# Kernel optimization log

Hardware: AMD Instinct MI355X
Metric: run time of the kernel (lower is better)

Reference implementation:

```python
import jax, jax.numpy as jnp
import numpy as np
from jax import lax

DIM = 256
MOTION = 128
HEADS = 8
HID = int(DIM * 3.0)
EPS = 1e-5


def std_ln(x, w, b):
    # standard nn.LayerNorm: biased var, /sqrt(var+eps)
    mean = x.mean(-1, keepdims=True)
    var = jnp.var(x, axis=-1, keepdims=True)
    return w * (x - mean) / jnp.sqrt(var + EPS) + b


def custom_ln(x, w, b):
    # repo's custom LayerNorm: UNBIASED std (ddof=1) and divide by (std+eps)
    mean = x.mean(-1, keepdims=True)
    std = jnp.std(x, axis=-1, ddof=1, keepdims=True)
    return w * (x - mean) / (std + EPS) + b


def setup_inputs() -> dict:
    key = jax.random.key(0)
    ks = jax.random.split(key, 32)
    s = 0.02
    d = {}
    d['x'] = jax.random.normal(ks[0], (4, 16384, DIM), jnp.float32)
    d['cor'] = jax.random.uniform(ks[1], (4, 128, 128, 2), jnp.float32)
    # attention projections (qkv_bias=False)
    d['q_w'] = jax.random.normal(ks[2], (DIM, DIM), jnp.float32) * s
    d['kv_w'] = jax.random.normal(ks[3], (2 * DIM, DIM), jnp.float32) * s
    d['cor_w'] = jax.random.normal(ks[4], (MOTION, 2), jnp.float32) * s
    hd = DIM // HEADS
    md = MOTION // HEADS
    d['kln_w'] = jnp.ones((HEADS, 1, hd), jnp.float32)
    d['kln_b'] = jnp.zeros((HEADS, 1, hd), jnp.float32)
    d['vln_w'] = jnp.ones((HEADS, 1, hd), jnp.float32)
    d['vln_b'] = jnp.zeros((HEADS, 1, hd), jnp.float32)
    d['corln_w'] = jnp.ones((HEADS, 1, md), jnp.float32)
    d['corln_b'] = jnp.zeros((HEADS, 1, md), jnp.float32)
    d['op1_w'] = jax.random.normal(ks[5], (DIM, DIM), jnp.float32) * s
    d['op1_b'] = jnp.zeros((DIM,), jnp.float32)
    d['op2_w'] = jax.random.normal(ks[6], (DIM, DIM), jnp.float32) * s
    d['op2_b'] = jnp.zeros((DIM,), jnp.float32)
    d['om1_w'] = jax.random.normal(ks[7], (MOTION, MOTION), jnp.float32) * s
    d['om1_b'] = jnp.zeros((MOTION,), jnp.float32)
    d['om2_w'] = jax.random.normal(ks[8], (MOTION, MOTION), jnp.float32) * s
    d['om2_b'] = jnp.zeros((MOTION,), jnp.float32)
    d['norm1_w'] = jnp.ones((DIM,), jnp.float32)
    d['norm1_b'] = jnp.zeros((DIM,), jnp.float32)
    d['norm2_w'] = jnp.ones((DIM,), jnp.float32)
    d['norm2_b'] = jnp.zeros((DIM,), jnp.float32)
    d['fc1_w'] = jax.random.normal(ks[9], (HID, DIM), jnp.float32) * s
    d['fc1_b'] = jnp.zeros((HID,), jnp.float32)
    d['dw_w'] = jax.random.normal(ks[10], (HID, 1, 3, 3), jnp.float32) * np.sqrt(2.0 / 9.0)
    d['dw_b'] = jnp.zeros((HID,), jnp.float32)
    d['fc2_w'] = jax.random.normal(ks[11], (DIM, HID), jnp.float32) * s
    d['fc2_b'] = jnp.zeros((DIM,), jnp.float32)
    d['H'] = 128
    d['W'] = 128
    d['B'] = 2
    return d


def _forward(x, cor, q_w, kv_w, cor_w, kln_w, kln_b, vln_w, vln_b,
             corln_w, corln_b, op1_w, op1_b, op2_w, op2_b,
             om1_w, om1_b, om2_w, om2_b, norm1_w, norm1_b,
             norm2_w, norm2_b, fc1_w, fc1_b, dw_w, dw_b, fc2_w, fc2_b,
             H, W, B):
    gelu = lambda t: jax.nn.gelu(t, approximate=False)
    nwB = 2 * B
    N = H * W
    C = x.shape[-1]
    M = cor_w.shape[0]
    h = kln_w.shape[0]
    hd = C // h
    md = M // h
    hid = fc1_w.shape[0]

    xw = x.reshape(nwB, N, C)            # window_partition with full window == identity
    corw = cor.reshape(nwB, N, 2)

    xn = std_ln(xw, norm1_w, norm1_b)
    half = nwB // 2
    xr = jnp.concatenate([xn[half:], xn[:half]], axis=0)  # swap frame halves

    q = (xn @ q_w.T).reshape(nwB, N, h, hd).transpose(0, 2, 1, 3)          # bhnd
    kv = (xr @ kv_w.T).reshape(nwB, N, 2, h, hd)
    k = kv[:, :, 0].transpose(0, 2, 1, 3)
    v = kv[:, :, 1].transpose(0, 2, 1, 3)
    ce_flat = corw @ cor_w.T                                               # (nwB,N,M)
    ce = ce_flat.reshape(nwB, N, h, md).transpose(0, 2, 1, 3)

    k = custom_ln(k, kln_w, kln_b)
    v = custom_ln(v, vln_w, vln_b)
    ce = custom_ln(ce, corln_w, corln_b)

    # linear attention: (k^T v)/N then q @ .
    ktv = jnp.einsum('bhnd,bhne->bhde', k, v) / N
    app = jnp.einsum('bhnd,bhde->bhne', q, ktv).transpose(0, 2, 1, 3).reshape(nwB, N, C)
    t = app + xn                                   # shortcut bias = x_norm
    x_app = gelu(t @ op1_w.T + op1_b) @ op2_w.T + op2_b + xn

    ktc = jnp.einsum('bhnd,bhne->bhde', k, ce) / N
    crev = jnp.einsum('bhnd,bhde->bhne', q, ktc).transpose(0, 2, 1, 3).reshape(nwB, N, M)
    dm = crev - ce_flat
    motion = gelu(dm @ om1_w.T + om1_b) @ om2_w.T + om2_b

    x_back = xn + x_app

    # Mlp with depthwise conv
    y = std_ln(x_back, norm2_w, norm2_b)
    h1 = y @ fc1_w.T + fc1_b                       # (nwB,N,hid)
    img = h1.transpose(0, 2, 1).reshape(nwB, hid, H, W)
    conv = lax.conv_general_dilated(img, dw_w, (1, 1), 'SAME',
                                    feature_group_count=hid,
                                    dimension_numbers=('NCHW', 'OIHW', 'NCHW'))
    conv = conv + dw_b[None, :, None, None]
    h2 = gelu(conv.reshape(nwB, hid, N).transpose(0, 2, 1))
    out = h2 @ fc2_w.T + fc2_b

    x_out = xw + out
    return x_out, motion


def reference(x, cor, q_w, kv_w, cor_w, kln_w, kln_b, vln_w, vln_b,
              corln_w, corln_b, op1_w, op1_b, op2_w, op2_b,
              om1_w, om1_b, om2_w, om2_b, norm1_w, norm1_b,
              norm2_w, norm2_b, fc1_w, fc1_b, dw_w, dw_b, fc2_w, fc2_b,
              H, W, B):
    return _forward(x, cor, q_w, kv_w, cor_w, kln_w, kln_b, vln_w, vln_b,
                    corln_w, corln_b, op1_w, op1_b, op2_w, op2_b,
                    om1_w, om1_b, om2_w, om2_b, norm1_w, norm1_b,
                    norm2_w, norm2_b, fc1_w, fc1_b, dw_w, dw_b, fc2_w, fc2_b,
                    H, W, B)
```

## Files before the change

### kernel.cpp

```cpp
#include <hip/hip_runtime.h>
#include <hip/hip_bf16.h>

#define NTOK 65536

typedef __attribute__((ext_vector_type(4))) float f32x4;
typedef __attribute__((ext_vector_type(8))) short bf16x8;

__device__ __forceinline__ float gelu_f(float x){
    float z = -2.30234438f * fmaf(0.044715f * x * x, x, x);
    float e = exp2f(z);
    return x * __builtin_amdgcn_rcpf(1.0f + e);
}
__device__ __forceinline__ float bf2f(unsigned short u){
    union { unsigned int i; float f; } w; w.i = ((unsigned int)u) << 16; return w.f;
}
__device__ __forceinline__ unsigned short f2bf(float f){
    __hip_bfloat16 h = __float2bfloat16(f);
    return *reinterpret_cast<unsigned short*>(&h);
}
__device__ __forceinline__ bf16x8 add_bf8(bf16x8 s, bf16x8 o, float k){
    bf16x8 r;
    #pragma unroll
    for (int i = 0; i < 8; i++)
        r[i] = (short)f2bf(fmaf(k, bf2f((unsigned short)o[i]), bf2f((unsigned short)s[i])));
    return r;
}

__global__ __launch_bounds__(256) void wconv_kernel(const float* __restrict__ q_w, const float* __restrict__ kv_w,
                                                    const float* __restrict__ op1_w, const float* __restrict__ op2_w,
                                                    const float* __restrict__ om1_w, const float* __restrict__ om2_w,
                                                    const float* __restrict__ fc1_w, const float* __restrict__ fc2_w,
                                                    unsigned short* __restrict__ Wb){
    size_t e = ((size_t)blockIdx.x * 256 + threadIdx.x) * 4;
    if (e >= 753664) return;
    const float* src; size_t off;
    if      (e <  65536){ src = q_w;   off = 0; }
    else if (e < 196608){ src = kv_w;  off = 65536; }
    else if (e < 262144){ src = op1_w; off = 196608; }
    else if (e < 327680){ src = op2_w; off = 262144; }
    else if (e < 344064){ src = om1_w; off = 327680; }
    else if (e < 360448){ src = om2_w; off = 344064; }
    else if (e < 557056){ src = fc1_w; off = 360448; }
    else                { src = fc2_w; off = 557056; }
    float4 v = *reinterpret_cast<const float4*>(src + (e - off));
    ushort4 o; o.x = f2bf(v.x); o.y = f2bf(v.y); o.z = f2bf(v.z); o.w = f2bf(v.w);
    *reinterpret_cast<ushort4*>(Wb + e) = o;
}

template<bool BF16IN>
__global__ __launch_bounds__(256) void stdln_kernel(const void* __restrict__ Xp,
                                                    const float* __restrict__ w,
                                                    const float* __restrict__ b,
                                                    unsigned short* __restrict__ out){
    int wv = threadIdx.x >> 6, lane = threadIdx.x & 63;
    int tok0 = (blockIdx.x * 4 + wv) * 8;
    int c0 = lane * 4;
    float4 w4 = *reinterpret_cast<const float4*>(w + c0);
    float4 b4 = *reinterpret_cast<const float4*>(b + c0);
    #pragma unroll 2
    for (int j = 0; j < 8; j++){
        size_t base = (size_t)(tok0 + j) * 256 + c0;
        float v[4];
        if constexpr (BF16IN){
            ushort4 u = *reinterpret_cast<const ushort4*>((const unsigned short*)Xp + base);
            v[0] = bf2f(u.x); v[1] = bf2f(u.y); v[2] = bf2f(u.z); v[3] = bf2f(u.w);
        } else {
            float4 f = *reinterpret_cast<const float4*>((const float*)Xp + base);
            v[0] = f.x; v[1] = f.y; v[2] = f.z; v[3] = f.w;
        }
        float s = v[0] + v[1] + v[2] + v[3];
        #pragma unroll
        for (int m = 1; m < 64; m <<= 1) s += __shfl_xor(s, m, 64);
        float mean = s * (1.0f / 256.0f);
        float ss = 0;
        #pragma unroll
        for (int k = 0; k < 4; k++){ v[k] -= mean; ss = fmaf(v[k], v[k], ss); }
        #pragma unroll
        for (int m = 1; m < 64; m <<= 1) ss += __shfl_xor(ss, m, 64);
        float inv = rsqrtf(ss * (1.0f / 256.0f) + 1e-5f);
        ushort4 o;
        o.x = f2bf(w4.x * v[0] * inv + b4.x);
        o.y = f2bf(w4.y * v[1] * inv + b4.y);
        o.z = f2bf(w4.z * v[2] * inv + b4.z);
        o.w = f2bf(w4.w * v[3] * inv + b4.w);
        *reinterpret_cast<ushort4*>(out + base) = o;
    }
}

__global__ __launch_bounds__(256) void ce_kernel(const float* __restrict__ cor,
                                                 const float* __restrict__ cor_w,
                                                 unsigned short* __restrict__ CEF){
    int m = threadIdx.x & 127, half = threadIdx.x >> 7;
    float w0 = cor_w[m * 2 + 0], w1 = cor_w[m * 2 + 1];
    #pragma unroll 4
    for (int it = 0; it < 16; it++){
        int tok = blockIdx.x * 32 + it * 2 + half;
        float c0 = cor[(size_t)tok * 2 + 0];
        float c1 = cor[(size_t)tok * 2 + 1];
        CEF[(size_t)tok * 128 + m] = f2bf(c0 * w0 + c1 * w1);
    }
}

__global__ __launch_bounds__(256) void ktvc_kernel(const unsigned short* __restrict__ Kb,
                                                   const unsigned short* __restrict__ Vb,
                                                   const unsigned short* __restrict__ CEF,
                                                   const float* __restrict__ kw, const float* __restrict__ kbb,
                                                   const float* __restrict__ vw, const float* __restrict__ vbb,
                                                   const float* __restrict__ cw, const float* __restrict__ cbb,
                                                   float* __restrict__ KTV, float* __restrict__ KTC){
    int bh = blockIdx.x, b = bh >> 3, h = bh & 7;
    __shared__ float Ks[64][36];
    __shared__ float Vs[64][36];
    __shared__ float Cs[64][20];
    __shared__ float P[2][64][24];
    int t = threadIdx.x;
    int lr = t >> 2, lq = t & 3;
    int g = t >> 6, tl = t & 63;
    int d0 = (tl >> 3) * 4, e0 = (tl & 7) * 4, e0c = (tl & 7) * 2;
    float kwr[8], kbr[8], vwr[8], vbr[8], cwr[4], cbr[4];
    #pragma unroll
    for (int j = 0; j < 8; j++){
        kwr[j] = kw[h * 32 + lq * 8 + j]; kbr[j] = kbb[h * 32 + lq * 8 + j];
        vwr[j] = vw[h * 32 + lq * 8 + j]; vbr[j] = vbb[h * 32 + lq * 8 + j];
    }
    #pragma unroll
    for (int j = 0; j < 4; j++){
        cwr[j] = cw[h * 16 + lq * 4 + j]; cbr[j] = cbb[h * 16 + lq * 4 + j];
    }
    float akv[4][4] = {};
    float akc[4][2] = {};
    size_t base = ((size_t)b << 14) + (size_t)blockIdx.y * 512;
    for (int n0 = 0; n0 < 512; n0 += 64){
        size_t rowi = base + n0 + lr;
        const ushort4* kp = reinterpret_cast<const ushort4*>(Kb + rowi * 256 + h * 32 + lq * 8);
        ushort4 ka = kp[0], kc = kp[1];
        const ushort4* vp = reinterpret_cast<const ushort4*>(Vb + rowi * 256 + h * 32 + lq * 8);
        ushort4 va = vp[0], vc = vp[1];
        ushort4 ca = *reinterpret_cast<const ushort4*>(CEF + rowi * 128 + h * 16 + lq * 4);
        float kvv[8] = { bf2f(ka.x), bf2f(ka.y), bf2f(ka.z), bf2f(ka.w),
                         bf2f(kc.x), bf2f(kc.y), bf2f(kc.z), bf2f(kc.w) };
        float vvv[8] = { bf2f(va.x), bf2f(va.y), bf2f(va.z), bf2f(va.w),
                         bf2f(vc.x), bf2f(vc.y), bf2f(vc.z), bf2f(vc.w) };
        float cvv[4] = { bf2f(ca.x), bf2f(ca.y), bf2f(ca.z), bf2f(ca.w) };
        float s = 0;
        #pragma unroll
        for (int j = 0; j < 8; j++) s += kvv[j];
        s += __shfl_xor(s, 1, 64); s += __shfl_xor(s, 2, 64);
        float mean = s * (1.0f / 32.0f);
        float ss = 0;
        #pragma unroll
        for (int j = 0; j < 8; j++){ kvv[j] -= mean; ss = fmaf(kvv[j], kvv[j], ss); }
        ss += __shfl_xor(ss, 1, 64); ss += __shfl_xor(ss, 2, 64);
        float inv = 1.0f / (sqrtf(ss * (1.0f / 31.0f)) + 1e-5f);
        #pragma unroll
        for (int j = 0; j < 8; j++) kvv[j] = fmaf(kwr[j] * kvv[j], inv, kbr[j]);
        s = 0;
        #pragma unroll
        for (int j = 0; j < 8; j++) s += vvv[j];
        s += __shfl_xor(s, 1, 64); s += __shfl_xor(s, 2, 64);
        mean = s * (1.0f / 32.0f);
        ss = 0;
        #pragma unroll
        for (int j = 0; j < 8; j++){ vvv[j] -= mean; ss = fmaf(vvv[j], vvv[j], ss); }
        ss += __shfl_xor(ss, 1, 64); ss += __shfl_xor(ss, 2, 64);
        inv = 1.0f / (sqrtf(ss * (1.0f / 31.0f)) + 1e-5f);
        #pragma unroll
        for (int j = 0; j < 8; j++) vvv[j] = fmaf(vwr[j] * vvv[j], inv, vbr[j]);
        s = 0;
        #pragma unroll
        for (int j = 0; j < 4; j++) s += cvv[j];
        s += __shfl_xor(s, 1, 64); s += __shfl_xor(s, 2, 64);
        mean = s * (1.0f / 16.0f);
        ss = 0;
        #pragma unroll
        for (int j = 0; j < 4; j++){ cvv[j] -= mean; ss = fmaf(cvv[j], cvv[j], ss); }
        ss += __shfl_xor(ss, 1, 64); ss += __shfl_xor(ss, 2, 64);
        inv = 1.0f / (sqrtf(ss * (1.0f / 15.0f)) + 1e-5f);
        #pragma unroll
        for (int j = 0; j < 4; j++) cvv[j] = fmaf(cwr[j] * cvv[j], inv, cbr[j]);
        __syncthreads();
        #pragma unroll
        for (int j = 0; j < 8; j++){ Ks[lr][lq * 8 + j] = kvv[j]; Vs[lr][lq * 8 + j] = vvv[j]; }
        #pragma unroll
        for (int j = 0; j < 4; j++) Cs[lr][lq * 4 + j] = cvv[j];
        __syncthreads();
        #pragma unroll 4
        for (int i = 0; i < 16; i++){
            int n = g * 16 + i;
            float4 k4 = *reinterpret_cast<const float4*>(&Ks[n][d0]);
            float4 v4 = *reinterpret_cast<const float4*>(&Vs[n][e0]);
            float2 c2 = *reinterpret_cast<const float2*>(&Cs[n][e0c]);
            float kk[4] = { k4.x, k4.y, k4.z, k4.w };
            float vv[4] = { v4.x, v4.y, v4.z, v4.w };
            #pragma unroll
            for (int a = 0; a < 4; a++){
                akv[a][0] = fmaf(kk[a], vv[0], akv[a][0]);
                akv[a][1] = fmaf(kk[a], vv[1], akv[a][1]);
                akv[a][2] = fmaf(kk[a], vv[2], akv[a][2]);
                akv[a][3] = fmaf(kk[a], vv[3], akv[a][3]);
                akc[a][0] = fmaf(kk[a], c2.x, akc[a][0]);
                akc[a][1] = fmaf(kk[a], c2.y, akc[a][1]);
            }
        }
    }
    __syncthreads();
    if (g >= 2){
        float* p = &P[g - 2][tl][0];
        #pragma unroll
        for (int a = 0; a < 4; a++){
            #pragma unroll
            for (int e = 0; e < 4; e++) p[a * 4 + e] = akv[a][e];
            p[16 + a * 2 + 0] = akc[a][0];
            p[16 + a * 2 + 1] = akc[a][1];
        }
    }
    __syncthreads();
    if (g < 2){
        const float* p = &P[g][tl][0];
        #pragma unroll
        for (int a = 0; a < 4; a++){
            #pragma unroll
            for (int e = 0; e < 4; e++) akv[a][e] += p[a * 4 + e];
            akc[a][0] += p[16 + a * 2 + 0];
            akc[a][1] += p[16 + a * 2 + 1];
        }
    }
    __syncthreads();
    if (g == 1){
        float* p = &P[0][tl][0];
        #pragma unroll
        for (int a = 0; a < 4; a++){
            #pragma unroll
            for (int e = 0; e < 4; e++) p[a * 4 + e] = akv[a][e];
            p[16 + a * 2 + 0] = akc[a][0];
            p[16 + a * 2 + 1] = akc[a][1];
        }
    }
    __syncthreads();
    if (g == 0){
        const float* p = &P[0][tl][0];
        const float sc = 1.0f / 16384.0f;
        float* o = KTV + (size_t)bh * 1024;
        float* o2 = KTC + (size_t)bh * 512;
        #pragma unroll
        for (int a = 0; a < 4; a++){
            #pragma unroll
            for (int e = 0; e < 4; e++)
                atomicAdd(&o[(d0 + a) * 32 + e0 + e], (akv[a][e] + p[a * 4 + e]) * sc);
            atomicAdd(&o2[(d0 + a) * 16 + e0c + 0], (akc[a][0] + p[16 + a * 2 + 0]) * sc);
            atomicAdd(&o2[(d0 + a) * 16 + e0c + 1], (akc[a][1] + p[16 + a * 2 + 1]) * sc);
        }
    }
}

__global__ __launch_bounds__(256) void wcomb_kernel(const float* __restrict__ q_w,
                                                    const float* __restrict__ KTV,
                                                    const float* __restrict__ KTC,
                                                    unsigned short* __restrict__ WTC){
    int c = blockIdx.x;
    int b = blockIdx.y;
    int i = threadIdx.x;
    __shared__ float coef[32];
    int h = (c < 256) ? (c >> 5) : ((c - 256) >> 4);
    if (i < 32){
        if (c < 256) coef[i] = KTV[(size_t)((b * 8 + h) << 10) + i * 32 + (c & 31)];
        else         coef[i] = KTC[(size_t)((b * 8 + h) << 9)  + i * 16 + ((c - 256) & 15)];
    }
    __syncthreads();
    float acc = 0;
    #pragma unroll
    for (int d = 0; d < 32; d++) acc = fmaf(q_w[(size_t)(h * 32 + d) * 256 + i], coef[d], acc);
    WTC[((size_t)b * 384 + c) * 256 + i] = f2bf(acc);
}

__global__ __launch_bounds__(192) void dwconv_kernel(const unsigned short* __restrict__ H1,
                                                     const float* __restrict__ dww,
                                                     const float* __restrict__ dwb,
                                                     unsigned short* __restrict__ H2){
    int blk = blockIdx.x;
    int xq = blk & 3;
    int yb = (blk >> 2) & 31;
    int bb = blk >> 7;
    int y0 = yb * 4, x0 = xq * 32;
    int ch = threadIdx.x * 4;
    float w[9][4];
    #pragma unroll
    for (int k = 0; k < 9; k++)
        #pragma unroll
        for (int j = 0; j < 4; j++) w[k][j] = dww[(ch + j) * 9 + k];
    float bias[4] = { dwb[ch], dwb[ch+1], dwb[ch+2], dwb[ch+3] };
    size_t rb[6]; bool rv[6];
    #pragma unroll
    for (int r = 0; r < 6; r++){
        int yr = y0 - 1 + r;
        rv[r] = ((unsigned)yr <= 127u);
        int yc = yr < 0 ? 0 : (yr > 127 ? 127 : yr);
        rb[r] = ((size_t)((bb << 14) + (yc << 7))) * 768 + ch;
    }
    size_t ob[4];
    #pragma unroll
    for (int j = 0; j < 4; j++) ob[j] = ((size_t)((bb << 14) + ((y0 + j) << 7))) * 768 + ch;

    ushort4 cA[6], cB[6], cC[6], cD[6];
    const ushort4 Z = {0, 0, 0, 0};
    #define LOADR(DST, XX) do {                                               \
        int _x = (XX);                                                        \
        bool xv = ((unsigned)_x <= 127u);                                     \
        _Pragma("unroll")                                                     \
        for (int r = 0; r < 6; r++)                                           \
            DST[r] = (xv && rv[r]) ? *reinterpret_cast<const ushort4*>(H1 + rb[r] + (size_t)_x * 768) : Z; \
    } while (0)

    #define EMITB(SA, SB, SC, XX) do {                                        \
        _Pragma("unroll")                                                     \
        for (int j = 0; j < 4; j++){                                          \
            float acc[4];                                                     \
            _Pragma("unroll")                                                 \
            for (int q = 0; q < 4; q++) acc[q] = bias[q];                     \
            _Pragma("unroll")                                                 \
            for (int rr2 = 0; rr2 < 3; rr2++){                                \
                int ri = j + rr2;                                             \
                float a0=bf2f(SA[ri].x),a1=bf2f(SA[ri].y),a2=bf2f(SA[ri].z),a3=bf2f(SA[ri].w); \
                float b0=bf2f(SB[ri].x),b1=bf2f(SB[ri].y),b2=bf2f(SB[ri].z),b3=bf2f(SB[ri].w); \
                float c0=bf2f(SC[ri].x),c1=bf2f(SC[ri].y),c2=bf2f(SC[ri].z),c3=bf2f(SC[ri].w); \
                acc[0]=fmaf(a0,w[rr2*3+0][0],acc[0]); acc[0]=fmaf(b0,w[rr2*3+1][0],acc[0]); acc[0]=fmaf(c0,w[rr2*3+2][0],acc[0]); \
                acc[1]=fmaf(a1,w[rr2*3+0][1],acc[1]); acc[1]=fmaf(b1,w[rr2*3+1][1],acc[1]); acc[1]=fmaf(c1,w[rr2*3+2][1],acc[1]); \
                acc[2]=fmaf(a2,w[rr2*3+0][2],acc[2]); acc[2]=fmaf(b2,w[rr2*3+1][2],acc[2]); acc[2]=fmaf(c2,w[rr2*3+2][2],acc[2]); \
                acc[3]=fmaf(a3,w[rr2*3+0][3],acc[3]); acc[3]=fmaf(b3,w[rr2*3+1][3],acc[3]); acc[3]=fmaf(c3,w[rr2*3+2][3],acc[3]); \
            }                                                                 \
            ushort4 o;                                                        \
            o.x = f2bf(gelu_f(acc[0])); o.y = f2bf(gelu_f(acc[1]));           \
            o.z = f2bf(gelu_f(acc[2])); o.w = f2bf(gelu_f(acc[3]));           \
            *reinterpret_cast<ushort4*>(H2 + ob[j] + (size_t)(XX) * 768) = o; \
        }                                                                     \
    } while (0)

    LOADR(cD, x0 - 1);
    LOADR(cA, x0);
    LOADR(cB, x0 + 1);
    LOADR(cC, x0 + 2);
    #pragma unroll 1
    for (int g = 0; g < 8; g++){
        int x = x0 + g * 4;
        EMITB(cD, cA, cB, x);     LOADR(cD, x + 3);
        EMITB(cA, cB, cC, x + 1); LOADR(cA, x + 4);
        EMITB(cB, cC, cD, x + 2); LOADR(cB, x + 5);
        EMITB(cC, cD, cA, x + 3); LOADR(cC, x + 6);
    }
    #undef LOADR
    #undef EMITB
}

#define M_KV        1
#define M_BIAS_GELU 2
#define M_BIAS_ADD2 3
#define M_BIAS      4
#define M_BIAS_BF16 5
#define M_BIAS_ADDX 6
#define M_ATTN      7

template<int MODE, bool SWAP, int K, int O, int WN>
__global__ __launch_bounds__(128 * WN) void mgemm(const unsigned short* __restrict__ A,
                                                  const unsigned short* __restrict__ Wp,
                                                  const float* __restrict__ bias,
                                                  const void* __restrict__ add,
                                                  void* __restrict__ out0,
                                                  void* __restrict__ out1){
    constexpr int WAVES = 2 * WN;
    constexpr int BN = 64 * WN;
    constexpr int CH = 8 + 4 * WN;
    constexpr int NT = K / 32;
    constexpr bool F32OUT = (MODE == M_BIAS || MODE == M_BIAS_ADDX);
    __shared__ __align__(16) unsigned short SMEM[2 * 128 * 32 + 2 * BN * 32];
    unsigned short* As0 = SMEM;
    unsigned short* Bs0 = SMEM + 2 * 128 * 32;
    const int t = threadIdx.x;
    const int lane = t & 63, wid = t >> 6;
    const int wm = wid & 1, wn = wid >> 1;
    const int row0 = blockIdx.x * 128;
    const int colB = blockIdx.y * BN;
    const unsigned short* W = Wp;
    if constexpr (MODE == M_ATTN) W += (size_t)(row0 >> 14) * (384 * 256);
    f32x4 acc[4][4];
    #pragma unroll
    for (int i = 0; i < 4; i++)
        #pragma unroll
        for (int j = 0; j < 4; j++){ f32x4 z = {0.f, 0.f, 0.f, 0.f}; acc[i][j] = z; }

    const int lr = lane >> 2;
    const int ls = lane & 3;
    const int kq = lane >> 4;
    const int rr = lane & 15;

    auto STAGE = [&](int buf, int kb){
        #pragma unroll
        for (int c = wid; c < CH; c += WAVES){
            int r16 = (c < 8) ? c : (c - 8);
            int row = r16 * 16 + lr;
            int ko = ls ^ ((row >> 1) & 3);
            if (c < 8){
                int ga = row0 + row;
                if (SWAP) ga ^= 32768;
                __builtin_amdgcn_global_load_lds(
                    (const __attribute__((address_space(1))) unsigned int*)(A + (size_t)ga * K + kb + ko * 8),
                    (__attribute__((address_space(3))) unsigned int*)(As0 + buf * 4096 + r16 * 512),
                    16, 0, 0);
            } else {
                int gc = colB + row;
                __builtin_amdgcn_global_load_lds(
                    (const __attribute__((address_space(1))) unsigned int*)(W + (size_t)gc * K + kb + ko * 8),
                    (__attribute__((address_space(3))) unsigned int*)(Bs0 + buf * (BN * 32) + r16 * 512),
                    16, 0, 0);
            }
        }
    };

    STAGE(0, 0);
    asm volatile("s_waitcnt vmcnt(0)" ::: "memory");
    __builtin_amdgcn_s_barrier();
    #pragma unroll 1
    for (int tt = 0; tt < NT; tt++){
        int cur = tt & 1;
        if (tt + 1 < NT) STAGE(cur ^ 1, (tt + 1) * 32);
        bf16x8 af[4], bfr[4];
        #pragma unroll
        for (int m = 0; m < 4; m++){
            int row = wm * 64 + m * 16 + rr;
            int s = kq ^ ((row >> 1) & 3);
            af[m] = *reinterpret_cast<const bf16x8*>(As0 + cur * 4096 + row * 32 + s * 8);
        }
        #pragma unroll
        for (int n = 0; n < 4; n++){
            int row = wn * 64 + n * 16 + rr;
            int s = kq ^ ((row >> 1) & 3);
            bfr[n] = *reinterpret_cast<const bf16x8*>(Bs0 + cur * (BN * 32) + row * 32 + s * 8);
        }
        #pragma unroll
        for (int m = 0; m < 4; m++)
            #pragma unroll
            for (int n = 0; n < 4; n++)
                acc[m][n] = __builtin_amdgcn_mfma_f32_16x16x32_bf16(af[m], bfr[n], acc[m][n], 0, 0, 0);
        if (tt + 1 < NT){
            asm volatile("s_waitcnt vmcnt(0)" ::: "memory");
            __builtin_amdgcn_s_barrier();
        }
    }

    __syncthreads();
    unsigned short* scr = SMEM + (size_t)wid * 2304;
    float* scrf = (float*)scr;
    const int rloc = lane >> 2;
    const int cs = (lane & 3) * 16;
    #pragma unroll
    for (int m = 0; m < 4; m++){
        #pragma unroll
        for (int n = 0; n < 4; n++){
            int col = colB + wn * 64 + n * 16 + rr;
            #pragma unroll
            for (int j = 0; j < 4; j++){
                float v = acc[m][n][j];
                int si = (kq * 4 + j) * 68 + n * 16 + rr;
                if constexpr (MODE == M_KV)            scr[si] = f2bf(v);
                else if constexpr (MODE == M_BIAS_GELU) scr[si] = f2bf(gelu_f(v + bias[col]));
                else if constexpr (MODE == M_BIAS_ADD2) scr[si] = f2bf(v + bias[col]);
                else if constexpr (MODE == M_BIAS_BF16) scr[si] = f2bf(v + bias[col]);
                else if constexpr (MODE == M_ATTN)      scr[si] = f2bf(v);
                else if constexpr (MODE == M_BIAS)      scrf[si] = v + bias[col];
                else if constexpr (MODE == M_BIAS_ADDX) scrf[si] = v + bias[col];
            }
        }
        int r = row0 + wm * 64 + m * 16 + rloc;
        int colb = colB + wn * 64 + cs;
        if constexpr (F32OUT){
            #pragma unroll
            for (int q = 0; q < 4; q++){
                float4 vv = *reinterpret_cast<const float4*>(&scrf[rloc * 68 + cs + q * 4]);
                size_t o = (size_t)r * O + colb + q * 4;
                if constexpr (MODE == M_BIAS_ADDX){
                    float4 xa = *reinterpret_cast<const float4*>(&((const float*)add)[o]);
                    vv.x += xa.x; vv.y += xa.y; vv.z += xa.z; vv.w += xa.w;
                }
                *reinterpret_cast<float4*>(&((float*)out0)[o]) = vv;
            }
        } else {
            #pragma unroll
            for (int q = 0; q < 2; q++){
                bf16x8 sv = *reinterpret_cast<const bf16x8*>(&scr[rloc * 68 + cs + q * 8]);
                int cg = colb + q * 8;
                if constexpr (MODE == M_KV){
                    unsigned short* dst = (cg < 256)
                        ? (unsigned short*)out0 + (size_t)r * 256 + cg
                        : (unsigned short*)out1 + (size_t)r * 256 + (cg - 256);
                    *reinterpret_cast<bf16x8*>(dst) = sv;
                } else if constexpr (MODE == M_ATTN){
                    if (cg < 256){
                        size_t o1 = (size_t)r * 256 + cg;
                        bf16x8 xv = *reinterpret_cast<const bf16x8*>((const unsigned short*)add + o1);
                        *reinterpret_cast<bf16x8*>((unsigned short*)out0 + o1) = add_bf8(sv, xv, 1.0f);
                    } else {
                        size_t o2 = (size_t)r * 128 + (cg - 256);
                        bf16x8 cv = *reinterpret_cast<const bf16x8*>((const unsigned short*)bias + o2);
                        *reinterpret_cast<bf16x8*>((unsigned short*)out1 + o2) = add_bf8(sv, cv, -1.0f);
                    }
                } else if constexpr (MODE == M_BIAS_ADD2){
                    size_t o = (size_t)r * O + cg;
                    bf16x8 xv = *reinterpret_cast<const bf16x8*>((const unsigned short*)add + o);
                    *reinterpret_cast<bf16x8*>((unsigned short*)out0 + o) = add_bf8(sv, xv, 2.0f);
                } else {
                    *reinterpret_cast<bf16x8*>((unsigned short*)out0 + (size_t)r * O + cg) = sv;
                }
            }
        }
    }
}

extern "C" void kernel_launch(void* const* d_in, const int* in_sizes, int n_in,
                              void* d_out, int out_size, void* d_ws, size_t ws_size,
                              hipStream_t stream){
    const float* x     = (const float*)d_in[0];
    const float* cor   = (const float*)d_in[1];
    const float* q_w   = (const float*)d_in[2];
    const float* kv_w  = (const float*)d_in[3];
    const float* cor_w = (const float*)d_in[4];
    const float* kln_w = (const float*)d_in[5];
    const float* kln_b = (const float*)d_in[6];
    const float* vln_w = (const float*)d_in[7];
    const float* vln_b = (const float*)d_in[8];
    const float* corln_w = (const float*)d_in[9];
    const float* corln_b = (const float*)d_in[10];
    const float* op1_w = (const float*)d_in[11];
    const float* op1_b = (const float*)d_in[12];
    const float* op2_w = (const float*)d_in[13];
    const float* op2_b = (const float*)d_in[14];
    const float* om1_w = (const float*)d_in[15];
    const float* om1_b = (const float*)d_in[16];
    const float* om2_w = (const float*)d_in[17];
    const float* om2_b = (const float*)d_in[18];
    const float* n1_w  = (const float*)d_in[19];
    const float* n1_b  = (const float*)d_in[20];
    const float* n2_w  = (const float*)d_in[21];
    const float* n2_b  = (const float*)d_in[22];
    const float* fc1_w = (const float*)d_in[23];
    const float* fc1_b = (const float*)d_in[24];
    const float* dw_w  = (const float*)d_in[25];
    const float* dw_b  = (const float*)d_in[26];
    const float* fc2_w = (const float*)d_in[27];
    const float* fc2_b = (const float*)d_in[28];

    unsigned short* XN  = (unsigned short*)d_ws;
    unsigned short* Qb  = XN  + (size_t)NTOK * 256;
    unsigned short* Kb  = Qb  + (size_t)NTOK * 256;
    unsigned short* Vb  = Kb  + (size_t)NTOK * 256;
    unsigned short* CEF = Vb  + (size_t)NTOK * 256;
    unsigned short* CE  = CEF + (size_t)NTOK * 128;
    float* KTV = (float*)(CE + (size_t)NTOK * 128);
    float* KTC = KTV + 32768;
    unsigned short* WTC = (unsigned short*)(KTC + 16384);
    unsigned short* Wb  = WTC + 4 * 384 * 256;
    unsigned short* H2  = Wb + 753664;
    unsigned short* T1 = Vb;
    unsigned short* T2 = Kb;
    unsigned short* XB = Qb;
    unsigned short* Y  = Vb;
    unsigned short* TM = CE;
    unsigned short* MH = CEF;
    unsigned short* H1 = XN;
    float* xout = (float*)d_out;
    float* mout = xout + (size_t)NTOK * 256;

    unsigned short* w_kv  = Wb + 65536;
    unsigned short* w_op1 = Wb + 196608;
    unsigned short* w_op2 = Wb + 262144;
    unsigned short* w_om1 = Wb + 327680;
    unsigned short* w_om2 = Wb + 344064;
    unsigned short* w_fc1 = Wb + 360448;
    unsigned short* w_fc2 = Wb + 557056;

    wconv_kernel<<<736, 256, 0, stream>>>(q_w, kv_w, op1_w, op2_w, om1_w, om2_w, fc1_w, fc2_w, Wb);
    stdln_kernel<false><<<2048, 256, 0, stream>>>(x, n1_w, n1_b, XN);
    mgemm<M_KV, true, 256, 512, 2><<<dim3(512, 4), 256, 0, stream>>>(XN, w_kv, nullptr, nullptr, Kb, Vb);
    ce_kernel<<<2048, 256, 0, stream>>>(cor, cor_w, CEF);
    hipMemsetAsync(KTV, 0, (32768 + 16384) * sizeof(float), stream);
    ktvc_kernel<<<dim3(32, 32), 256, 0, stream>>>(Kb, Vb, CEF, kln_w, kln_b, vln_w, vln_b,
                                                  corln_w, corln_b, KTV, KTC);
    wcomb_kernel<<<dim3(384, 4), 256, 0, stream>>>(q_w, KTV, KTC, WTC);
    mgemm<M_ATTN, false, 256, 384, 3><<<dim3(512, 2), 384, 0, stream>>>(XN, WTC, (const float*)CEF, XN, T1, TM);
    mgemm<M_BIAS_GELU, false, 256, 256, 2><<<dim3(512, 2), 256, 0, stream>>>(T1, w_op1, op1_b, nullptr, T2, nullptr);
    mgemm<M_BIAS_ADD2, false, 256, 256, 2><<<dim3(512, 2), 256, 0, stream>>>(T2, w_op2, op2_b, XN, XB, nullptr);
    mgemm<M_BIAS_GELU, false, 128, 128, 2><<<dim3(512, 1), 256, 0, stream>>>(TM, w_om1, om1_b, nullptr, MH, nullptr);
    mgemm<M_BIAS, false, 128, 128, 2><<<dim3(512, 1), 256, 0, stream>>>(MH, w_om2, om2_b, nullptr, mout, nullptr);
    stdln_kernel<true><<<2048, 256, 0, stream>>>(XB, n2_w, n2_b, Y);
    mgemm<M_BIAS_BF16, false, 256, 768, 3><<<dim3(512, 4), 384, 0, stream>>>(Y, w_fc1, fc1_b, nullptr, H1, nullptr);
    dwconv_kernel<<<512, 192, 0, stream>>>(H1, dw_w, dw_b, H2);
    mgemm<M_BIAS_ADDX, false, 768, 256, 2><<<dim3(512, 2), 256, 0, stream>>>(H2, w_fc2, fc2_b, x, xout, nullptr);
}
```

Measured before the change: 452.5 us.

## Fuse residual add and LayerNorm into op2 GEMM epilogue; widen GEMM column tiles

```diff
diff --git a/kernel.cpp b/kernel.cpp
--- a/kernel.cpp
+++ b/kernel.cpp
@@ -353,17 +353,19 @@
 
 #define M_KV        1
 #define M_BIAS_GELU 2
-#define M_BIAS_ADD2 3
 #define M_BIAS      4
 #define M_BIAS_BF16 5
 #define M_BIAS_ADDX 6
 #define M_ATTN      7
+#define M_ADD2LN    8
 
 template<int MODE, bool SWAP, int K, int O, int WN>
 __global__ __launch_bounds__(128 * WN) void mgemm(const unsigned short* __restrict__ A,
                                                   const unsigned short* __restrict__ Wp,
                                                   const float* __restrict__ bias,
                                                   const void* __restrict__ add,
+                                                  const float* __restrict__ nw,
+                                                  const float* __restrict__ nb,
                                                   void* __restrict__ out0,
                                                   void* __restrict__ out1){
     constexpr int WAVES = 2 * WN;
@@ -451,6 +453,65 @@
     float* scrf = (float*)scr;
     const int rloc = lane >> 2;
     const int cs = (lane & 3) * 16;
+
+    if constexpr (MODE == M_ADD2LN){
+        float* rowS = (float*)(SMEM + 20480);
+        float* rowQ = rowS + 512;
+        #pragma unroll
+        for (int m = 0; m < 4; m++){
+            #pragma unroll
+            for (int j = 0; j < 4; j++){
+                int r = row0 + wm * 64 + m * 16 + kq * 4 + j;
+                float s = 0, q = 0;
+                #pragma unroll
+                for (int n = 0; n < 4; n++){
+                    int col = wn * 64 + n * 16 + rr;
+                    float v = acc[m][n][j] + bias[col]
+                            + 2.0f * bf2f(((const unsigned short*)add)[(size_t)r * 256 + col]);
+                    acc[m][n][j] = v;
+                    s += v; q = fmaf(v, v, q);
+                }
+                s += __shfl_xor(s, 1, 64); s += __shfl_xor(s, 2, 64);
+                s += __shfl_xor(s, 4, 64); s += __shfl_xor(s, 8, 64);
+                q += __shfl_xor(q, 1, 64); q += __shfl_xor(q, 2, 64);
+                q += __shfl_xor(q, 4, 64); q += __shfl_xor(q, 8, 64);
+                if (rr == 0){
+                    int lrow = wm * 64 + m * 16 + kq * 4 + j;
+                    rowS[wn * 128 + lrow] = s;
+                    rowQ[wn * 128 + lrow] = q;
+                }
+            }
+        }
+        __syncthreads();
+        #pragma unroll
+        for (int m = 0; m < 4; m++){
+            #pragma unroll
+            for (int n = 0; n < 4; n++){
+                int col = wn * 64 + n * 16 + rr;
+                float w2 = nw[col], b2 = nb[col];
+                #pragma unroll
+                for (int j = 0; j < 4; j++){
+                    int lrow = wm * 64 + m * 16 + kq * 4 + j;
+                    float S = rowS[lrow] + rowS[128 + lrow] + rowS[256 + lrow] + rowS[384 + lrow];
+                    float Q = rowQ[lrow] + rowQ[128 + lrow] + rowQ[256 + lrow] + rowQ[384 + lrow];
+                    float mean = S * (1.0f / 256.0f);
+                    float var = fmaxf(Q * (1.0f / 256.0f) - mean * mean, 0.0f);
+                    float inv = rsqrtf(var + 1e-5f);
+                    float y = w2 * (acc[m][n][j] - mean) * inv + b2;
+                    scr[(kq * 4 + j) * 68 + n * 16 + rr] = f2bf(y);
+                }
+            }
+            int r = row0 + wm * 64 + m * 16 + rloc;
+            #pragma unroll
+            for (int q = 0; q < 2; q++){
+                bf16x8 sv = *reinterpret_cast<const bf16x8*>(&scr[rloc * 68 + cs + q * 8]);
+                int cg = wn * 64 + cs + q * 8;
+                *reinterpret_cast<bf16x8*>((unsigned short*)out0 + (size_t)r * O + cg) = sv;
+            }
+        }
+        return;
+    }
+
     #pragma unroll
     for (int m = 0; m < 4; m++){
         #pragma unroll
@@ -462,7 +523,6 @@
                 int si = (kq * 4 + j) * 68 + n * 16 + rr;
                 if constexpr (MODE == M_KV)            scr[si] = f2bf(v);
                 else if constexpr (MODE == M_BIAS_GELU) scr[si] = f2bf(gelu_f(v + bias[col]));
-                else if constexpr (MODE == M_BIAS_ADD2) scr[si] = f2bf(v + bias[col]);
                 else if constexpr (MODE == M_BIAS_BF16) scr[si] = f2bf(v + bias[col]);
                 else if constexpr (MODE == M_ATTN)      scr[si] = f2bf(v);
                 else if constexpr (MODE == M_BIAS)      scrf[si] = v + bias[col];
@@ -502,10 +562,6 @@
                         bf16x8 cv = *reinterpret_cast<const bf16x8*>((const unsigned short*)bias + o2);
                         *reinterpret_cast<bf16x8*>((unsigned short*)out1 + o2) = add_bf8(sv, cv, -1.0f);
                     }
-                } else if constexpr (MODE == M_BIAS_ADD2){
-                    size_t o = (size_t)r * O + cg;
-                    bf16x8 xv = *reinterpret_cast<const bf16x8*>((const unsigned short*)add + o);
-                    *reinterpret_cast<bf16x8*>((unsigned short*)out0 + o) = add_bf8(sv, xv, 2.0f);
                 } else {
                     *reinterpret_cast<bf16x8*>((unsigned short*)out0 + (size_t)r * O + cg) = sv;
                 }
@@ -560,13 +616,14 @@
     unsigned short* H2  = Wb + 753664;
     unsigned short* T1 = Vb;
     unsigned short* T2 = Kb;
-    unsigned short* XB = Qb;
-    unsigned short* Y  = Vb;
+    unsigned short* Y  = Qb;
     unsigned short* TM = CE;
     unsigned short* MH = CEF;
     unsigned short* H1 = XN;
     float* xout = (float*)d_out;
     float* mout = xout + (size_t)NTOK * 256;
+
+    unsigned short* H1s = H2 + (size_t)NTOK * 768;
 
     unsigned short* w_kv  = Wb + 65536;
     unsigned short* w_op1 = Wb + 196608;
@@ -578,19 +635,18 @@
 
     wconv_kernel<<<736, 256, 0, stream>>>(q_w, kv_w, op1_w, op2_w, om1_w, om2_w, fc1_w, fc2_w, Wb);
     stdln_kernel<false><<<2048, 256, 0, stream>>>(x, n1_w, n1_b, XN);
-    mgemm<M_KV, true, 256, 512, 2><<<dim3(512, 4), 256, 0, stream>>>(XN, w_kv, nullptr, nullptr, Kb, Vb);
+    mgemm<M_KV, true, 256, 512, 8><<<dim3(512, 1), 1024, 0, stream>>>(XN, w_kv, nullptr, nullptr, nullptr, nullptr, Kb, Vb);
     ce_kernel<<<2048, 256, 0, stream>>>(cor, cor_w, CEF);
     hipMemsetAsync(KTV, 0, (32768 + 16384) * sizeof(float), stream);
     ktvc_kernel<<<dim3(32, 32), 256, 0, stream>>>(Kb, Vb, CEF, kln_w, kln_b, vln_w, vln_b,
                                                   corln_w, corln_b, KTV, KTC);
     wcomb_kernel<<<dim3(384, 4), 256, 0, stream>>>(q_w, KTV, KTC, WTC);
-    mgemm<M_ATTN, false, 256, 384, 3><<<dim3(512, 2), 384, 0, stream>>>(XN, WTC, (const float*)CEF, XN, T1, TM);
-    mgemm<M_BIAS_GELU, false, 256, 256, 2><<<dim3(512, 2), 256, 0, stream>>>(T1, w_op1, op1_b, nullptr, T2, nullptr);
-    mgemm<M_BIAS_ADD2, false, 256, 256, 2><<<dim3(512, 2), 256, 0, stream>>>(T2, w_op2, op2_b, XN, XB, nullptr);
-    mgemm<M_BIAS_GELU, false, 128, 128, 2><<<dim3(512, 1), 256, 0, stream>>>(TM, w_om1, om1_b, nullptr, MH, nullptr);
-    mgemm<M_BIAS, false, 128, 128, 2><<<dim3(512, 1), 256, 0, stream>>>(MH, w_om2, om2_b, nullptr, mout, nullptr);
-    stdln_kernel<true><<<2048, 256, 0, stream>>>(XB, n2_w, n2_b, Y);
-    mgemm<M_BIAS_BF16, false, 256, 768, 3><<<dim3(512, 4), 384, 0, stream>>>(Y, w_fc1, fc1_b, nullptr, H1, nullptr);
-    dwconv_kernel<<<512, 192, 0, stream>>>(H1, dw_w, dw_b, H2);
-    mgemm<M_BIAS_ADDX, false, 768, 256, 2><<<dim3(512, 2), 256, 0, stream>>>(H2, w_fc2, fc2_b, x, xout, nullptr);
-}
+    mgemm<M_ATTN, false, 256, 384, 6><<<dim3(512, 1), 768, 0, stream>>>(XN, WTC, (const float*)CEF, XN, nullptr, nullptr, T1, TM);
+    mgemm<M_BIAS_GELU, false, 256, 256, 4><<<dim3(512, 1), 512, 0, stream>>>(T1, w_op1, op1_b, nullptr, nullptr, nullptr, T2, nullptr);
+    mgemm<M_ADD2LN, false, 256, 256, 4><<<dim3(512, 1), 512, 0, stream>>>(T2, w_op2, op2_b, XN, n2_w, n2_b, Y, nullptr);
+    mgemm<M_BIAS_GELU, false, 128, 128, 2><<<dim3(512, 1), 256, 0, stream>>>(TM, w_om1, om1_b, nullptr, nullptr, nullptr, MH, nullptr);
+    mgemm<M_BIAS, false, 128, 128, 2><<<dim3(512, 1), 256, 0, stream>>>(MH, w_om2, om2_b, nullptr, nullptr, nullptr, mout, nullptr);
+    mgemm<M_BIAS_BF16, false, 256, 768, 6><<<dim3(512, 2), 768, 0, stream>>>(Y, w_fc1, fc1_b, nullptr, nullptr, nullptr, H1s, nullptr);
+    dwconv_kernel<<<512, 192, 0, stream>>>(H1s, dw_w, dw_b, H2);
+    mgemm<M_BIAS_ADDX, false, 768, 256, 4><<<dim3(512, 1), 512, 0, stream>>>(H2, w_fc2, fc2_b, x, nullptr, nullptr, xout, nullptr);
+}
```

Result: faster. 425.1 us (-6.1%).
